# Optimization experiments

Hardware: AMD Instinct MI355X
Metric: run time of the kernel (lower is better)

Reference implementation:

```python
import jax, jax.numpy as jnp
import numpy as np

DILATIONS = [2 ** i for i in range(9)] * 3  # 27 layers
RD, SD, QD = 32, 512, 256


def conv1d(x, w, b, dilation=1, padding=0):
    # x: [B,C,T], w: [O,I,K], b: [O]
    out = jax.lax.conv_general_dilated(
        x, w, window_strides=(1,), padding=[(padding, padding)],
        rhs_dilation=(dilation,), dimension_numbers=('NCH', 'OIH', 'NCH'))
    return out + b[None, :, None]


def setup_inputs() -> dict:
    key = jax.random.key(0)
    ks = jax.random.split(key, 16)
    T = 131072
    L = len(DILATIONS)
    s = 0.05
    inp = {
        'x': jax.random.normal(ks[0], (1, 1, T), dtype=jnp.float32),
        'Wc': jax.random.normal(ks[1], (RD, 1, 3), dtype=jnp.float32) * s,
        'bc': jnp.zeros((RD,), dtype=jnp.float32),
        'Wt': jax.random.normal(ks[2], (L, RD, RD, 3), dtype=jnp.float32) * s,
        'bt': jnp.zeros((L, RD), dtype=jnp.float32),
        'Ws': jax.random.normal(ks[3], (L, RD, RD, 3), dtype=jnp.float32) * s,
        'bs': jnp.zeros((L, RD), dtype=jnp.float32),
        'Wskip': jax.random.normal(ks[4], (L, SD, RD, 1), dtype=jnp.float32) * s,
        'bskip': jnp.zeros((L, SD), dtype=jnp.float32),
        'Wdense': jax.random.normal(ks[5], (L, RD, RD, 1), dtype=jnp.float32) * s,
        'bdense': jnp.zeros((L, RD), dtype=jnp.float32),
        'Wp1': jax.random.normal(ks[6], (SD, SD, 1), dtype=jnp.float32) * s,
        'bp1': jnp.zeros((SD,), dtype=jnp.float32),
        'Wp2': jax.random.normal(ks[7], (QD, SD, 1), dtype=jnp.float32) * s,
        'bp2': jnp.zeros((QD,), dtype=jnp.float32),
    }
    return inp


def reference(x, Wc, bc, Wt, bt, Ws, bs, Wskip, bskip, Wdense, bdense, Wp1, bp1, Wp2, bp2):
    # causal conv: kernel 3, padding 1 (same length)
    x = conv1d(x, Wc, bc, dilation=1, padding=1)  # [1, RD, T]
    skip = jnp.zeros((1, SD, x.shape[2]), dtype=jnp.float32)
    for i, d in enumerate(DILATIONS):
        xin = x
        g = jnp.tanh(conv1d(x, Wt[i], bt[i], d, d)) * jax.nn.sigmoid(conv1d(x, Ws[i], bs[i], d, d))
        skip = skip + conv1d(g, Wskip[i], bskip[i])
        x = conv1d(g, Wdense[i], bdense[i]) + xin
    # NOTE: the original applies F.relu(x) on the residual path but then
    # overwrites x with the skip-path result, so that relu is dead code.
    out = conv1d(jax.nn.relu(conv1d(skip, Wp1, bp1)), Wp2, bp2)  # [1, QD, T]
    return jax.nn.log_softmax(out, axis=1)
```

## Files before the change

kernel.cpp:

```cpp
#include <hip/hip_runtime.h>

#define T_LEN 131072
#define RD 32
#define SD 512
#define QD 256
#define NL 27
#define KTOT (NL * RD)

typedef __attribute__((ext_vector_type(8))) short short8;
typedef __attribute__((ext_vector_type(4))) float floatx4;

__device__ __forceinline__ unsigned short f2bf(float f) {
    union { float f; unsigned int i; } v; v.f = f;
    unsigned int r = v.i + 0x7fffu + ((v.i >> 16) & 1u);
    return (unsigned short)(r >> 16);
}

__device__ __forceinline__ void gload_lds16(const void* g, void* l) {
    __builtin_amdgcn_global_load_lds(
        (const __attribute__((address_space(1))) unsigned int*)g,
        (__attribute__((address_space(3))) unsigned int*)l, 16, 0, 0);
}

__global__ __launch_bounds__(256)
void k_conv_init(const float* __restrict__ x, const float* __restrict__ Wc,
                 const float* __restrict__ bc, float* __restrict__ xout,
                 unsigned short* __restrict__ xoutb)
{
    const int t = blockIdx.x * 256 + threadIdx.x;
    const float xm = (t > 0) ? x[t - 1] : 0.f;
    const float x0 = x[t];
    const float xp = (t < T_LEN - 1) ? x[t + 1] : 0.f;
    float* row = xout + (size_t)t * RD;
    unsigned short* rowb = xoutb + (size_t)t * RD;
#pragma unroll
    for (int o = 0; o < RD; ++o) {
        const float v = bc[o] + Wc[o * 3 + 0] * xm + Wc[o * 3 + 1] * x0 + Wc[o * 3 + 2] * xp;
        row[o] = v;
        rowb[o] = f2bf(v);
    }
}

__global__ __launch_bounds__(256)
void k_wprep(const float* __restrict__ Wt, const float* __restrict__ Ws,
             const float* __restrict__ Wd,
             unsigned short* __restrict__ Wg, unsigned short* __restrict__ Wdb)
{
    const int idx = blockIdx.x * 256 + threadIdx.x;
    const int n1 = NL * 64 * 96;
    const int n2 = NL * RD * RD;
    if (idx < n1) {
        const int l = idx / (64 * 96);
        const int rem = idx % (64 * 96);
        const int m = rem / 96;
        const int k = rem % 96;
        const int j = k / 32;
        const int c = k % 32;
        float v;
        if (m < 32) v = Wt[(((size_t)l * RD + m) * RD + c) * 3 + j];
        else        v = Ws[(((size_t)l * RD + (m - 32)) * RD + c) * 3 + j];
        Wg[idx] = f2bf(v);
    } else if (idx < n1 + n2) {
        const int i2 = idx - n1;
        Wdb[i2] = f2bf(Wd[i2]);
    }
}

__global__ __launch_bounds__(256)
void k_layer_mfma(const float* __restrict__ xin, const unsigned short* __restrict__ xinb,
                  float* __restrict__ xout, unsigned short* __restrict__ xoutb,
                  unsigned short* __restrict__ Gt,
                  const unsigned short* __restrict__ Wg,
                  const unsigned short* __restrict__ Wdb,
                  const float* __restrict__ bt, const float* __restrict__ bs,
                  const float* __restrict__ bd, int d, int layer)
{
    __shared__ unsigned short gtile[128 * 32];
    const int tid = threadIdx.x;
    const int lane = tid & 63;
    const int w = tid >> 6;
    const int quad = lane >> 4;
    const int l16 = lane & 15;
    const int tbase = blockIdx.x * 128 + w * 32;

    short8 afr[3][4];
#pragma unroll
    for (int j = 0; j < 3; ++j)
#pragma unroll
        for (int mt = 0; mt < 4; ++mt)
            afr[j][mt] = *reinterpret_cast<const short8*>(
                Wg + (size_t)(mt * 16 + l16) * 96 + j * 32 + quad * 8);

    floatx4 acc[4][2];
    const floatx4 vzero = {0.f, 0.f, 0.f, 0.f};
#pragma unroll
    for (int mt = 0; mt < 4; ++mt)
#pragma unroll
        for (int nt = 0; nt < 2; ++nt) acc[mt][nt] = vzero;

#pragma unroll
    for (int nt = 0; nt < 2; ++nt) {
        const int t = tbase + nt * 16 + l16;
#pragma unroll
        for (int j = 0; j < 3; ++j) {
            const int tt = t + (j - 1) * d;
            short8 b;
            if (tt >= 0 && tt < T_LEN) {
                b = *reinterpret_cast<const short8*>(xinb + (size_t)tt * RD + quad * 8);
            } else {
#pragma unroll
                for (int i = 0; i < 8; ++i) b[i] = 0;
            }
#pragma unroll
            for (int mt = 0; mt < 4; ++mt)
                acc[mt][nt] = __builtin_amdgcn_mfma_f32_16x16x32_bf16(afr[j][mt], b, acc[mt][nt], 0, 0, 0);
        }
    }

#pragma unroll
    for (int nt = 0; nt < 2; ++nt) {
        const int t = tbase + nt * 16 + l16;
        const int tloc = w * 32 + nt * 16 + l16;
#pragma unroll
        for (int pair = 0; pair < 2; ++pair) {
            const floatx4 bt4 = *reinterpret_cast<const floatx4*>(bt + pair * 16 + quad * 4);
            const floatx4 bs4 = *reinterpret_cast<const floatx4*>(bs + pair * 16 + quad * 4);
            ushort4 u;
            unsigned short us[4];
#pragma unroll
            for (int r = 0; r < 4; ++r) {
                const float a1 = acc[pair][nt][r] + bt4[r];
                const float a2 = acc[2 + pair][nt][r] + bs4[r];
                const float th = 1.f - __fdividef(2.f, __expf(2.f * a1) + 1.f);
                const float sg = __fdividef(1.f, 1.f + __expf(-a2));
                us[r] = f2bf(th * sg);
            }
            u.x = us[0]; u.y = us[1]; u.z = us[2]; u.w = us[3];
            const int cbase = pair * 16 + quad * 4;
            *reinterpret_cast<ushort4*>(&gtile[tloc * 32 + cbase]) = u;
            *reinterpret_cast<ushort4*>(Gt + (size_t)t * KTOT + layer * 32 + cbase) = u;
        }
    }

    __syncthreads();

    short8 ad[2];
#pragma unroll
    for (int mt = 0; mt < 2; ++mt)
        ad[mt] = *reinterpret_cast<const short8*>(Wdb + (size_t)(mt * 16 + l16) * 32 + quad * 8);

#pragma unroll
    for (int nt = 0; nt < 2; ++nt) {
        const int t = tbase + nt * 16 + l16;
        const int tloc = w * 32 + nt * 16 + l16;
        const short8 bg = *reinterpret_cast<const short8*>(&gtile[tloc * 32 + quad * 8]);
#pragma unroll
        for (int mt = 0; mt < 2; ++mt) {
            const floatx4 a2 = __builtin_amdgcn_mfma_f32_16x16x32_bf16(ad[mt], bg, vzero, 0, 0, 0);
            const int m = mt * 16 + quad * 4;
            const floatx4 bd4 = *reinterpret_cast<const floatx4*>(bd + m);
            const floatx4 xi = *reinterpret_cast<const floatx4*>(xin + (size_t)t * RD + m);
            floatx4 o;
            ushort4 ob;
            o[0] = a2[0] + bd4[0] + xi[0]; ob.x = f2bf(o[0]);
            o[1] = a2[1] + bd4[1] + xi[1]; ob.y = f2bf(o[1]);
            o[2] = a2[2] + bd4[2] + xi[2]; ob.z = f2bf(o[2]);
            o[3] = a2[3] + bd4[3] + xi[3]; ob.w = f2bf(o[3]);
            *reinterpret_cast<floatx4*>(xout + (size_t)t * RD + m) = o;
            *reinterpret_cast<ushort4*>(xoutb + (size_t)t * RD + m) = ob;
        }
    }
}

__global__ __launch_bounds__(256)
void k_wcomb(const float* __restrict__ Wp1, const float* __restrict__ Wskip,
             unsigned short* __restrict__ Wcomb)
{
    const int idx = blockIdx.x * 256 + threadIdx.x;
    if (idx >= SD * KTOT) return;
    const int m = idx / KTOT;
    const int k = idx % KTOT;
    const int l = k / RD;
    const int c = k % RD;
    const float* wp1r = Wp1 + (size_t)m * SD;
    const float* wsk = Wskip + (size_t)l * SD * RD + c;
    float acc = 0.f;
    for (int j = 0; j < SD; ++j) acc += wp1r[j] * wsk[(size_t)j * RD];
    Wcomb[idx] = f2bf(acc);
}

__global__ __launch_bounds__(512)
void k_hbias(const float* __restrict__ Wp1, const float* __restrict__ bp1,
             const float* __restrict__ bskip, float* __restrict__ hbias)
{
    __shared__ float sb[SD];
    const int tid = threadIdx.x;
    float s = 0.f;
    for (int l = 0; l < NL; ++l) s += bskip[l * SD + tid];
    sb[tid] = s;
    __syncthreads();
    float acc = bp1[tid];
    const float* r = Wp1 + (size_t)tid * SD;
    for (int j = 0; j < SD; ++j) acc += r[j] * sb[j];
    hbias[tid] = acc;
}

__global__ __launch_bounds__(256)
void k_cvt(const float* __restrict__ src, unsigned short* __restrict__ dst, int n)
{
    const int i = blockIdx.x * 256 + threadIdx.x;
    if (i < n) dst[i] = f2bf(src[i]);
}

__global__ __launch_bounds__(256)
void k_gemm1(const unsigned short* __restrict__ A,
             const unsigned short* __restrict__ B,
             const float* __restrict__ hbias,
             unsigned short* __restrict__ ht)
{
    __shared__ unsigned short ldsA[128 * 32];
    __shared__ unsigned short ldsB[128 * 32];
    const int tid = threadIdx.x;
    const int lane = tid & 63;
    const int w = tid >> 6;
    const int wm = w & 1;
    const int wn = w >> 1;
    const int quad = lane >> 4;
    const int l16 = lane & 15;

    const int g = blockIdx.x;
    const int m0 = ((g >> 3) & 3) * 128;
    const int n0 = ((g & 7) + 8 * (g >> 5)) * 128;

    const int r4 = lane >> 2;
    const int c4 = lane & 3;
    const int srcc = c4 ^ ((r4 >> 1) & 3);
    const int swz = (l16 >> 1) & 3;

    floatx4 acc[4][4];
    const floatx4 vzero = {0.f, 0.f, 0.f, 0.f};
#pragma unroll
    for (int mt = 0; mt < 4; ++mt)
#pragma unroll
        for (int nt = 0; nt < 4; ++nt) acc[mt][nt] = vzero;

    for (int kc = 0; kc < KTOT / 32; ++kc) {
        const int k0 = kc * 32;
#pragma unroll
        for (int c = 0; c < 2; ++c) {
            const int row = w * 32 + c * 16;
            gload_lds16(A + (size_t)(m0 + row + r4) * KTOT + k0 + srcc * 8,
                        &ldsA[(size_t)row * 32]);
            gload_lds16(B + (size_t)(n0 + row + r4) * KTOT + k0 + srcc * 8,
                        &ldsB[(size_t)row * 32]);
        }
        __syncthreads();

        short8 afr[4], bfr[4];
#pragma unroll
        for (int mt = 0; mt < 4; ++mt)
            afr[mt] = *reinterpret_cast<const short8*>(
                &ldsA[(wm * 64 + mt * 16 + l16) * 32 + (quad ^ swz) * 8]);
#pragma unroll
        for (int nt = 0; nt < 4; ++nt)
            bfr[nt] = *reinterpret_cast<const short8*>(
                &ldsB[(wn * 64 + nt * 16 + l16) * 32 + (quad ^ swz) * 8]);
#pragma unroll
        for (int mt = 0; mt < 4; ++mt)
#pragma unroll
            for (int nt = 0; nt < 4; ++nt)
                acc[mt][nt] = __builtin_amdgcn_mfma_f32_16x16x32_bf16(afr[mt], bfr[nt], acc[mt][nt], 0, 0, 0);
        __syncthreads();
    }

#pragma unroll
    for (int mt = 0; mt < 4; ++mt) {
        const int m = m0 + wm * 64 + mt * 16 + quad * 4;
        const floatx4 hb = *reinterpret_cast<const floatx4*>(hbias + m);
#pragma unroll
        for (int nt = 0; nt < 4; ++nt) {
            const int t = n0 + wn * 64 + nt * 16 + l16;
            ushort4 st;
            float v;
            v = acc[mt][nt][0] + hb[0]; st.x = f2bf(v > 0.f ? v : 0.f);
            v = acc[mt][nt][1] + hb[1]; st.y = f2bf(v > 0.f ? v : 0.f);
            v = acc[mt][nt][2] + hb[2]; st.z = f2bf(v > 0.f ? v : 0.f);
            v = acc[mt][nt][3] + hb[3]; st.w = f2bf(v > 0.f ? v : 0.f);
            *reinterpret_cast<ushort4*>(ht + (size_t)t * SD + m) = st;
        }
    }
}

__global__ __launch_bounds__(256)
void k_gemm2_lsm(const unsigned short* __restrict__ A,
                 const unsigned short* __restrict__ B,
                 const float* __restrict__ bp2,
                 float* __restrict__ out)
{
    __shared__ unsigned short ldsB[64 * 32];
    __shared__ float redmax[4 * 16 * 16];
    __shared__ float redsum[4 * 16 * 16];
    const int tid = threadIdx.x;
    const int lane = tid & 63;
    const int w = tid >> 6;
    const int quad = lane >> 4;
    const int l16 = lane & 15;
    const int m0 = w * 64;
    const int n0 = blockIdx.x * 64;

    const int r4 = lane >> 2;
    const int c4 = lane & 3;
    const int srcc = c4 ^ ((r4 >> 1) & 3);
    const int swz = (l16 >> 1) & 3;

    const unsigned short* ab[4];
#pragma unroll
    for (int mt = 0; mt < 4; ++mt)
        ab[mt] = A + (size_t)(m0 + mt * 16 + l16) * SD + quad * 8;

    floatx4 acc[4][4];
    const floatx4 vzero = {0.f, 0.f, 0.f, 0.f};
#pragma unroll
    for (int mt = 0; mt < 4; ++mt)
#pragma unroll
        for (int nt = 0; nt < 4; ++nt) acc[mt][nt] = vzero;

    for (int kc = 0; kc < SD / 32; ++kc) {
        const int k0 = kc * 32;
        gload_lds16(B + (size_t)(n0 + w * 16 + r4) * SD + k0 + srcc * 8,
                    &ldsB[(size_t)(w * 16) * 32]);
        short8 afr[4];
#pragma unroll
        for (int mt = 0; mt < 4; ++mt)
            afr[mt] = *reinterpret_cast<const short8*>(ab[mt] + k0);
        __syncthreads();

        short8 bfr[4];
#pragma unroll
        for (int nt = 0; nt < 4; ++nt)
            bfr[nt] = *reinterpret_cast<const short8*>(
                &ldsB[(nt * 16 + l16) * 32 + (quad ^ swz) * 8]);
#pragma unroll
        for (int mt = 0; mt < 4; ++mt)
#pragma unroll
            for (int nt = 0; nt < 4; ++nt)
                acc[mt][nt] = __builtin_amdgcn_mfma_f32_16x16x32_bf16(
                    afr[mt], bfr[nt], acc[mt][nt], 0, 0, 0);
        __syncthreads();
    }

#pragma unroll
    for (int mt = 0; mt < 4; ++mt) {
        const int mb = m0 + mt * 16 + quad * 4;
        const floatx4 bz = *reinterpret_cast<const floatx4*>(bp2 + mb);
#pragma unroll
        for (int nt = 0; nt < 4; ++nt)
#pragma unroll
            for (int j = 0; j < 4; ++j) acc[mt][nt][j] += bz[j];
    }

#pragma unroll
    for (int nt = 0; nt < 4; ++nt) {
        float lm = -1e30f;
#pragma unroll
        for (int mt = 0; mt < 4; ++mt)
#pragma unroll
            for (int j = 0; j < 4; ++j) lm = fmaxf(lm, acc[mt][nt][j]);
        redmax[nt * 256 + l16 * 16 + w * 4 + quad] = lm;
    }
    __syncthreads();

    float lse[4];
#pragma unroll
    for (int nt = 0; nt < 4; ++nt) {
        float gm = -1e30f;
#pragma unroll
        for (int i = 0; i < 16; ++i) gm = fmaxf(gm, redmax[nt * 256 + l16 * 16 + i]);
        float ls = 0.f;
#pragma unroll
        for (int mt = 0; mt < 4; ++mt)
#pragma unroll
            for (int j = 0; j < 4; ++j) ls += __expf(acc[mt][nt][j] - gm);
        redsum[nt * 256 + l16 * 16 + w * 4 + quad] = ls;
        lse[nt] = gm;
    }
    __syncthreads();

#pragma unroll
    for (int nt = 0; nt < 4; ++nt) {
        float tot = 0.f;
#pragma unroll
        for (int i = 0; i < 16; ++i) tot += redsum[nt * 256 + l16 * 16 + i];
        lse[nt] = lse[nt] + __logf(tot);
    }

#pragma unroll
    for (int mt = 0; mt < 4; ++mt) {
        const int mb = m0 + mt * 16 + quad * 4;
#pragma unroll
        for (int nt = 0; nt < 4; ++nt) {
            const int t = n0 + nt * 16 + l16;
#pragma unroll
            for (int j = 0; j < 4; ++j)
                out[(size_t)(mb + j) * T_LEN + t] = acc[mt][nt][j] - lse[nt];
        }
    }
}

extern "C" void kernel_launch(void* const* d_in, const int* in_sizes, int n_in,
                              void* d_out, int out_size, void* d_ws, size_t ws_size,
                              hipStream_t stream)
{
    (void)in_sizes; (void)n_in; (void)out_size; (void)ws_size;
    const float* x     = (const float*)d_in[0];
    const float* Wc    = (const float*)d_in[1];
    const float* bc    = (const float*)d_in[2];
    const float* Wt    = (const float*)d_in[3];
    const float* bt    = (const float*)d_in[4];
    const float* Ws    = (const float*)d_in[5];
    const float* bs    = (const float*)d_in[6];
    const float* Wskip = (const float*)d_in[7];
    const float* bskip = (const float*)d_in[8];
    const float* Wd    = (const float*)d_in[9];
    const float* bd    = (const float*)d_in[10];
    const float* Wp1   = (const float*)d_in[11];
    const float* bp1   = (const float*)d_in[12];
    const float* Wp2   = (const float*)d_in[13];
    const float* bp2   = (const float*)d_in[14];
    float* out = (float*)d_out;

    char* p = (char*)d_ws;
    unsigned short* Gt = (unsigned short*)p;    p += (size_t)T_LEN * KTOT * 2;
    unsigned short* ht = (unsigned short*)p;    p += (size_t)T_LEN * SD * 2;
    unsigned short* Wcomb = (unsigned short*)p; p += (size_t)SD * KTOT * 2;
    unsigned short* Wp2b = (unsigned short*)p;  p += (size_t)QD * SD * 2;
    unsigned short* Wg = (unsigned short*)p;    p += (size_t)NL * 64 * 96 * 2;
    unsigned short* Wdb = (unsigned short*)p;   p += (size_t)NL * RD * RD * 2;
    float* hbias = (float*)p;                   p += (size_t)SD * 4;

    char* q = (char*)ht;
    float* xa = (float*)q;                      q += (size_t)T_LEN * RD * 4;
    float* xb = (float*)q;                      q += (size_t)T_LEN * RD * 4;
    unsigned short* xba = (unsigned short*)q;   q += (size_t)T_LEN * RD * 2;
    unsigned short* xbb = (unsigned short*)q;   q += (size_t)T_LEN * RD * 2;

    k_wcomb<<<(SD * KTOT + 255) / 256, 256, 0, stream>>>(Wp1, Wskip, Wcomb);
    k_hbias<<<1, 512, 0, stream>>>(Wp1, bp1, bskip, hbias);
    k_cvt<<<(QD * SD + 255) / 256, 256, 0, stream>>>(Wp2, Wp2b, QD * SD);
    {
        const int nprep = NL * 64 * 96 + NL * RD * RD;
        k_wprep<<<(nprep + 255) / 256, 256, 0, stream>>>(Wt, Ws, Wd, Wg, Wdb);
    }
    k_conv_init<<<T_LEN / 256, 256, 0, stream>>>(x, Wc, bc, xa, xba);

    static const int dil[NL] = {1, 2, 4, 8, 16, 32, 64, 128, 256,
                                1, 2, 4, 8, 16, 32, 64, 128, 256,
                                1, 2, 4, 8, 16, 32, 64, 128, 256};
    const float* cur = xa;
    const unsigned short* curb = xba;
    float* nxt = xb;
    unsigned short* nxtb = xbb;
    for (int i = 0; i < NL; ++i) {
        k_layer_mfma<<<T_LEN / 128, 256, 0, stream>>>(
            cur, curb, nxt, nxtb, Gt,
            Wg + (size_t)i * 64 * 96,
            Wdb + (size_t)i * RD * RD,
            bt + (size_t)i * RD,
            bs + (size_t)i * RD,
            bd + (size_t)i * RD,
            dil[i], i);
        float* tf = (float*)cur; cur = nxt; nxt = tf;
        unsigned short* tb = (unsigned short*)curb; curb = nxtb; nxtb = tb;
    }

    k_gemm1<<<4 * (T_LEN / 128), 256, 0, stream>>>(Wcomb, Gt, hbias, ht);
    k_gemm2_lsm<<<T_LEN / 64, 256, 0, stream>>>(Wp2b, ht, bp2, out);
}
```

Before: 1.057 ms.

## Double-buffer LDS tiles in both GEMM kernels to overlap global loads with MFMA

Both projection GEMMs now keep two LDS buffers. The next K-chunk is prefetched with direct global-to-LDS loads while the current chunk feeds the MFMAs. The __syncthreads pairs are replaced by explicit vmcnt/lgkmcnt waits and raw s_barrier, which removes the load-latency stall each iteration. LDS usage doubles, which may reduce occupancy, and the hand-written waitcnt counts must match the number of outstanding loads exactly.

Measured after the change: 1.092 ms. 1.03x slower.

```diff
diff --git a/kernel.cpp b/kernel.cpp
--- a/kernel.cpp
+++ b/kernel.cpp
@@ -218,8 +218,8 @@
              const float* __restrict__ hbias,
              unsigned short* __restrict__ ht)
 {
-    __shared__ unsigned short ldsA[128 * 32];
-    __shared__ unsigned short ldsB[128 * 32];
+    __shared__ unsigned short ldsA[2][128 * 32];
+    __shared__ unsigned short ldsB[2][128 * 32];
     const int tid = threadIdx.x;
     const int lane = tid & 63;
     const int w = tid >> 6;
@@ -244,33 +244,50 @@
 #pragma unroll
         for (int nt = 0; nt < 4; ++nt) acc[mt][nt] = vzero;
 
+    const unsigned short* pA = A + (size_t)(m0 + r4) * KTOT + srcc * 8;
+    const unsigned short* pB = B + (size_t)(n0 + r4) * KTOT + srcc * 8;
+
+#pragma unroll
+    for (int c = 0; c < 2; ++c) {
+        const int row = w * 32 + c * 16;
+        gload_lds16(pA + (size_t)row * KTOT, &ldsA[0][row * 32]);
+        gload_lds16(pB + (size_t)row * KTOT, &ldsB[0][row * 32]);
+    }
+
     for (int kc = 0; kc < KTOT / 32; ++kc) {
-        const int k0 = kc * 32;
-#pragma unroll
-        for (int c = 0; c < 2; ++c) {
-            const int row = w * 32 + c * 16;
-            gload_lds16(A + (size_t)(m0 + row + r4) * KTOT + k0 + srcc * 8,
-                        &ldsA[(size_t)row * 32]);
-            gload_lds16(B + (size_t)(n0 + row + r4) * KTOT + k0 + srcc * 8,
-                        &ldsB[(size_t)row * 32]);
-        }
-        __syncthreads();
+        const int cur = kc & 1;
+        if (kc + 1 < KTOT / 32) {
+            const int k0n = (kc + 1) * 32;
+#pragma unroll
+            for (int c = 0; c < 2; ++c) {
+                const int row = w * 32 + c * 16;
+                gload_lds16(pA + (size_t)row * KTOT + k0n, &ldsA[cur ^ 1][row * 32]);
+                gload_lds16(pB + (size_t)row * KTOT + k0n, &ldsB[cur ^ 1][row * 32]);
+            }
+            asm volatile("s_waitcnt vmcnt(4)" ::: "memory");
+        } else {
+            asm volatile("s_waitcnt vmcnt(0)" ::: "memory");
+        }
+        __builtin_amdgcn_s_barrier();
+        asm volatile("" ::: "memory");
 
         short8 afr[4], bfr[4];
 #pragma unroll
         for (int mt = 0; mt < 4; ++mt)
             afr[mt] = *reinterpret_cast<const short8*>(
-                &ldsA[(wm * 64 + mt * 16 + l16) * 32 + (quad ^ swz) * 8]);
+                &ldsA[cur][(wm * 64 + mt * 16 + l16) * 32 + (quad ^ swz) * 8]);
 #pragma unroll
         for (int nt = 0; nt < 4; ++nt)
             bfr[nt] = *reinterpret_cast<const short8*>(
-                &ldsB[(wn * 64 + nt * 16 + l16) * 32 + (quad ^ swz) * 8]);
+                &ldsB[cur][(wn * 64 + nt * 16 + l16) * 32 + (quad ^ swz) * 8]);
 #pragma unroll
         for (int mt = 0; mt < 4; ++mt)
 #pragma unroll
             for (int nt = 0; nt < 4; ++nt)
                 acc[mt][nt] = __builtin_amdgcn_mfma_f32_16x16x32_bf16(afr[mt], bfr[nt], acc[mt][nt], 0, 0, 0);
-        __syncthreads();
+
+        asm volatile("s_waitcnt lgkmcnt(0)" ::: "memory");
+        __builtin_amdgcn_s_barrier();
     }
 
 #pragma unroll
@@ -297,7 +314,7 @@
                  const float* __restrict__ bp2,
                  float* __restrict__ out)
 {
-    __shared__ unsigned short ldsB[64 * 32];
+    __shared__ unsigned short ldsB[2][64 * 32];
     __shared__ float redmax[4 * 16 * 16];
     __shared__ float redsum[4 * 16 * 16];
     const int tid = threadIdx.x;
@@ -318,6 +335,8 @@
     for (int mt = 0; mt < 4; ++mt)
         ab[mt] = A + (size_t)(m0 + mt * 16 + l16) * SD + quad * 8;
 
+    const unsigned short* pB = B + (size_t)(n0 + w * 16 + r4) * SD + srcc * 8;
+
     floatx4 acc[4][4];
     const floatx4 vzero = {0.f, 0.f, 0.f, 0.f};
 #pragma unroll
@@ -325,28 +344,41 @@
 #pragma unroll
         for (int nt = 0; nt < 4; ++nt) acc[mt][nt] = vzero;
 
+    gload_lds16(pB, &ldsB[0][(w * 16) * 32]);
+
     for (int kc = 0; kc < SD / 32; ++kc) {
+        const int cur = kc & 1;
         const int k0 = kc * 32;
-        gload_lds16(B + (size_t)(n0 + w * 16 + r4) * SD + k0 + srcc * 8,
-                    &ldsB[(size_t)(w * 16) * 32]);
+
         short8 afr[4];
 #pragma unroll
         for (int mt = 0; mt < 4; ++mt)
             afr[mt] = *reinterpret_cast<const short8*>(ab[mt] + k0);
-        __syncthreads();
+        asm volatile("" ::: "memory");
+
+        if (kc + 1 < SD / 32) {
+            gload_lds16(pB + (kc + 1) * 32, &ldsB[cur ^ 1][(w * 16) * 32]);
+            asm volatile("s_waitcnt vmcnt(1)" ::: "memory");
+        } else {
+            asm volatile("s_waitcnt vmcnt(0)" ::: "memory");
+        }
+        __builtin_amdgcn_s_barrier();
+        asm volatile("" ::: "memory");
 
         short8 bfr[4];
 #pragma unroll
         for (int nt = 0; nt < 4; ++nt)
             bfr[nt] = *reinterpret_cast<const short8*>(
-                &ldsB[(nt * 16 + l16) * 32 + (quad ^ swz) * 8]);
+                &ldsB[cur][(nt * 16 + l16) * 32 + (quad ^ swz) * 8]);
 #pragma unroll
         for (int mt = 0; mt < 4; ++mt)
 #pragma unroll
             for (int nt = 0; nt < 4; ++nt)
                 acc[mt][nt] = __builtin_amdgcn_mfma_f32_16x16x32_bf16(
                     afr[mt], bfr[nt], acc[mt][nt], 0, 0, 0);
-        __syncthreads();
+
+        asm volatile("s_waitcnt lgkmcnt(0)" ::: "memory");
+        __builtin_amdgcn_s_barrier();
     }
 
 #pragma unroll
```

## Store gate and hidden buffers in K-chunked layout and drop bf16 residual copy

Applied to the files above, without the earlier changes.

The gate buffer Gt, the combined weight Wcomb and the hidden buffer ht move from row-major [T][K] to a chunked [K/32][T][32] layout. Each GEMM k-step now reads a contiguous block instead of strided 64-byte pieces, and the layer kernels write contiguous 64-byte rows per layer. The separate bf16 copy of the residual stream is removed, and each layer converts the fp32 input to bf16 on the fly. That trades more fp32 read traffic (twice the bytes for the dilated taps) for fewer writes.

Result: faster. 1.029 ms (-2.6%).

```diff
diff --git a/kernel.cpp b/kernel.cpp
--- a/kernel.cpp
+++ b/kernel.cpp
@@ -24,20 +24,16 @@
 
 __global__ __launch_bounds__(256)
 void k_conv_init(const float* __restrict__ x, const float* __restrict__ Wc,
-                 const float* __restrict__ bc, float* __restrict__ xout,
-                 unsigned short* __restrict__ xoutb)
+                 const float* __restrict__ bc, float* __restrict__ xout)
 {
     const int t = blockIdx.x * 256 + threadIdx.x;
     const float xm = (t > 0) ? x[t - 1] : 0.f;
     const float x0 = x[t];
     const float xp = (t < T_LEN - 1) ? x[t + 1] : 0.f;
     float* row = xout + (size_t)t * RD;
-    unsigned short* rowb = xoutb + (size_t)t * RD;
 #pragma unroll
     for (int o = 0; o < RD; ++o) {
-        const float v = bc[o] + Wc[o * 3 + 0] * xm + Wc[o * 3 + 1] * x0 + Wc[o * 3 + 2] * xp;
-        row[o] = v;
-        rowb[o] = f2bf(v);
+        row[o] = bc[o] + Wc[o * 3 + 0] * xm + Wc[o * 3 + 1] * x0 + Wc[o * 3 + 2] * xp;
     }
 }
 
@@ -67,8 +63,8 @@
 }
 
 __global__ __launch_bounds__(256)
-void k_layer_mfma(const float* __restrict__ xin, const unsigned short* __restrict__ xinb,
-                  float* __restrict__ xout, unsigned short* __restrict__ xoutb,
+void k_layer_mfma(const float* __restrict__ xin,
+                  float* __restrict__ xout,
                   unsigned short* __restrict__ Gt,
                   const unsigned short* __restrict__ Wg,
                   const unsigned short* __restrict__ Wdb,
@@ -106,7 +102,14 @@
             const int tt = t + (j - 1) * d;
             short8 b;
             if (tt >= 0 && tt < T_LEN) {
-                b = *reinterpret_cast<const short8*>(xinb + (size_t)tt * RD + quad * 8);
+                const float* src = xin + (size_t)tt * RD + quad * 8;
+                const floatx4 f0 = *reinterpret_cast<const floatx4*>(src);
+                const floatx4 f1 = *reinterpret_cast<const floatx4*>(src + 4);
+#pragma unroll
+                for (int i = 0; i < 4; ++i) {
+                    b[i] = (short)f2bf(f0[i]);
+                    b[4 + i] = (short)f2bf(f1[i]);
+                }
             } else {
 #pragma unroll
                 for (int i = 0; i < 8; ++i) b[i] = 0;
@@ -138,7 +141,8 @@
             u.x = us[0]; u.y = us[1]; u.z = us[2]; u.w = us[3];
             const int cbase = pair * 16 + quad * 4;
             *reinterpret_cast<ushort4*>(&gtile[tloc * 32 + cbase]) = u;
-            *reinterpret_cast<ushort4*>(Gt + (size_t)t * KTOT + layer * 32 + cbase) = u;
+            *reinterpret_cast<ushort4*>(
+                Gt + ((size_t)layer * T_LEN + t) * RD + cbase) = u;
         }
     }
 
@@ -161,13 +165,11 @@
             const floatx4 bd4 = *reinterpret_cast<const floatx4*>(bd + m);
             const floatx4 xi = *reinterpret_cast<const floatx4*>(xin + (size_t)t * RD + m);
             floatx4 o;
-            ushort4 ob;
-            o[0] = a2[0] + bd4[0] + xi[0]; ob.x = f2bf(o[0]);
-            o[1] = a2[1] + bd4[1] + xi[1]; ob.y = f2bf(o[1]);
-            o[2] = a2[2] + bd4[2] + xi[2]; ob.z = f2bf(o[2]);
-            o[3] = a2[3] + bd4[3] + xi[3]; ob.w = f2bf(o[3]);
+            o[0] = a2[0] + bd4[0] + xi[0];
+            o[1] = a2[1] + bd4[1] + xi[1];
+            o[2] = a2[2] + bd4[2] + xi[2];
+            o[3] = a2[3] + bd4[3] + xi[3];
             *reinterpret_cast<floatx4*>(xout + (size_t)t * RD + m) = o;
-            *reinterpret_cast<ushort4*>(xoutb + (size_t)t * RD + m) = ob;
         }
     }
 }
@@ -186,7 +188,7 @@
     const float* wsk = Wskip + (size_t)l * SD * RD + c;
     float acc = 0.f;
     for (int j = 0; j < SD; ++j) acc += wp1r[j] * wsk[(size_t)j * RD];
-    Wcomb[idx] = f2bf(acc);
+    Wcomb[((size_t)l * SD + m) * RD + c] = f2bf(acc);
 }
 
 __global__ __launch_bounds__(512)
@@ -244,15 +246,15 @@
 #pragma unroll
         for (int nt = 0; nt < 4; ++nt) acc[mt][nt] = vzero;
 
+    const unsigned short* pA = A + (size_t)(m0 + r4) * RD + srcc * 8;
+    const unsigned short* pB = B + (size_t)(n0 + r4) * RD + srcc * 8;
+
     for (int kc = 0; kc < KTOT / 32; ++kc) {
-        const int k0 = kc * 32;
 #pragma unroll
         for (int c = 0; c < 2; ++c) {
             const int row = w * 32 + c * 16;
-            gload_lds16(A + (size_t)(m0 + row + r4) * KTOT + k0 + srcc * 8,
-                        &ldsA[(size_t)row * 32]);
-            gload_lds16(B + (size_t)(n0 + row + r4) * KTOT + k0 + srcc * 8,
-                        &ldsB[(size_t)row * 32]);
+            gload_lds16(pA + ((size_t)kc * SD + row) * RD, &ldsA[(size_t)row * 32]);
+            gload_lds16(pB + ((size_t)kc * T_LEN + row) * RD, &ldsB[(size_t)row * 32]);
         }
         __syncthreads();
 
@@ -277,6 +279,8 @@
     for (int mt = 0; mt < 4; ++mt) {
         const int m = m0 + wm * 64 + mt * 16 + quad * 4;
         const floatx4 hb = *reinterpret_cast<const floatx4*>(hbias + m);
+        const size_t chunkbase = (size_t)(m >> 5) * T_LEN;
+        const int mc = m & 31;
 #pragma unroll
         for (int nt = 0; nt < 4; ++nt) {
             const int t = n0 + wn * 64 + nt * 16 + l16;
@@ -286,7 +290,7 @@
             v = acc[mt][nt][1] + hb[1]; st.y = f2bf(v > 0.f ? v : 0.f);
             v = acc[mt][nt][2] + hb[2]; st.z = f2bf(v > 0.f ? v : 0.f);
             v = acc[mt][nt][3] + hb[3]; st.w = f2bf(v > 0.f ? v : 0.f);
-            *reinterpret_cast<ushort4*>(ht + (size_t)t * SD + m) = st;
+            *reinterpret_cast<ushort4*>(ht + (chunkbase + t) * RD + mc) = st;
         }
     }
 }
@@ -318,6 +322,8 @@
     for (int mt = 0; mt < 4; ++mt)
         ab[mt] = A + (size_t)(m0 + mt * 16 + l16) * SD + quad * 8;
 
+    const unsigned short* pB = B + (size_t)(n0 + w * 16 + r4) * RD + srcc * 8;
+
     floatx4 acc[4][4];
     const floatx4 vzero = {0.f, 0.f, 0.f, 0.f};
 #pragma unroll
@@ -327,8 +333,7 @@
 
     for (int kc = 0; kc < SD / 32; ++kc) {
         const int k0 = kc * 32;
-        gload_lds16(B + (size_t)(n0 + w * 16 + r4) * SD + k0 + srcc * 8,
-                    &ldsB[(size_t)(w * 16) * 32]);
+        gload_lds16(pB + (size_t)kc * T_LEN * RD, &ldsB[(size_t)(w * 16) * 32]);
         short8 afr[4];
 #pragma unroll
         for (int mt = 0; mt < 4; ++mt)
@@ -441,8 +446,6 @@
     char* q = (char*)ht;
     float* xa = (float*)q;                      q += (size_t)T_LEN * RD * 4;
     float* xb = (float*)q;                      q += (size_t)T_LEN * RD * 4;
-    unsigned short* xba = (unsigned short*)q;   q += (size_t)T_LEN * RD * 2;
-    unsigned short* xbb = (unsigned short*)q;   q += (size_t)T_LEN * RD * 2;
 
     k_wcomb<<<(SD * KTOT + 255) / 256, 256, 0, stream>>>(Wp1, Wskip, Wcomb);
     k_hbias<<<1, 512, 0, stream>>>(Wp1, bp1, bskip, hbias);
@@ -451,18 +454,16 @@
         const int nprep = NL * 64 * 96 + NL * RD * RD;
         k_wprep<<<(nprep + 255) / 256, 256, 0, stream>>>(Wt, Ws, Wd, Wg, Wdb);
     }
-    k_conv_init<<<T_LEN / 256, 256, 0, stream>>>(x, Wc, bc, xa, xba);
+    k_conv_init<<<T_LEN / 256, 256, 0, stream>>>(x, Wc, bc, xa);
 
     static const int dil[NL] = {1, 2, 4, 8, 16, 32, 64, 128, 256,
                                 1, 2, 4, 8, 16, 32, 64, 128, 256,
                                 1, 2, 4, 8, 16, 32, 64, 128, 256};
     const float* cur = xa;
-    const unsigned short* curb = xba;
     float* nxt = xb;
-    unsigned short* nxtb = xbb;
     for (int i = 0; i < NL; ++i) {
         k_layer_mfma<<<T_LEN / 128, 256, 0, stream>>>(
-            cur, curb, nxt, nxtb, Gt,
+            cur, nxt, Gt,
             Wg + (size_t)i * 64 * 96,
             Wdb + (size_t)i * RD * RD,
             bt + (size_t)i * RD,
@@ -470,7 +471,6 @@
             bd + (size_t)i * RD,
             dil[i], i);
         float* tf = (float*)cur; cur = nxt; nxt = tf;
-        unsigned short* tb = (unsigned short*)curb; curb = nxtb; nxtb = tb;
     }
 
     k_gemm1<<<4 * (T_LEN / 128), 256, 0, stream>>>(Wcomb, Gt, hbias, ht);
```
